# Performance work log

Measured on AMD Instinct MI355X. Metric: run time of the kernel, lower is better.

Reference implementation:

```python
import jax, jax.numpy as jnp
import numpy as np
from jax import lax

I, H, O, S = 1024, 1024, 32000, 2048


def setup_inputs() -> dict:
    key = jax.random.key(0)
    ks = jax.random.split(key, 7)
    s = 1.0 / np.sqrt(H)
    return {
        "x": jax.random.normal(ks[0], (1, S, I), jnp.float32),
        "W_ih": jax.random.uniform(ks[1], (H, I), jnp.float32, -s, s),
        "W_hh": jax.random.uniform(ks[2], (H, H), jnp.float32, -s, s),
        "b_ih": jax.random.uniform(ks[3], (H,), jnp.float32, -s, s),
        "b_hh": jax.random.uniform(ks[4], (H,), jnp.float32, -s, s),
        "W_fc": jax.random.uniform(ks[5], (O, H), jnp.float32, -s, s),
        "b_fc": jax.random.uniform(ks[6], (O,), jnp.float32, -s, s),
    }


def reference(x, W_ih, W_hh, b_ih, b_hh, W_fc, b_fc):
    # Precompute input projection for all timesteps in one GEMM: [s, H]
    xp = jnp.einsum('si,hi->sh', x[0], W_ih) + b_ih + b_hh
    h0 = jnp.zeros((W_hh.shape[0],), x.dtype)

    def step(h, xt):
        h_new = jnp.tanh(xt + h @ W_hh.T)
        return h_new, h_new

    _, hs = lax.scan(step, h0, xp)  # hs: [s, H]
    # Linear head over all timesteps: [s, O]
    return hs @ W_fc.T + b_fc
```

## Files before the change

### kernel.cpp

```cpp
#include <hip/hip_runtime.h>
#include <math.h>

typedef _Float16 f16;
typedef f16 f16x2 __attribute__((ext_vector_type(2)));
typedef f16 f16x4 __attribute__((ext_vector_type(4)));
typedef f16 f16x8 __attribute__((ext_vector_type(8)));
typedef float f32x4 __attribute__((ext_vector_type(4)));

#define HDIM 1024
#define SEQ  2048
#define NBLK 16
#define NGWK 240
#define RPB  64
#define NTIL 4000

__global__ void k_clear(unsigned long long* __restrict__ p, int n,
                        unsigned* __restrict__ sR, int nr,
                        unsigned* __restrict__ sG, int ng) {
  int stride = gridDim.x * blockDim.x;
  int id = blockIdx.x * blockDim.x + threadIdx.x;
  for (int i = id; i < n; i += stride) p[i] = 0ULL;
  for (int i = id; i < nr; i += stride) sR[i] = 0u;
  for (int i = id; i < ng; i += stride) sG[i] = 0u;
}

__global__ void k_cvt(const float* __restrict__ in, f16* __restrict__ out, int n4) {
  int stride = gridDim.x * blockDim.x;
  for (int i = blockIdx.x * blockDim.x + threadIdx.x; i < n4; i += stride) {
    float4 v = ((const float4*)in)[i];
    f16x4 o = { (f16)v.x, (f16)v.y, (f16)v.z, (f16)v.w };
    ((f16x4*)out)[i] = o;
  }
}

__global__ void k_bias(const float* __restrict__ a, const float* __restrict__ b,
                       float* __restrict__ o) {
  int i = blockIdx.x * blockDim.x + threadIdx.x;
  if (i < HDIM) o[i] = a[i] + b[i];
}

__global__ __launch_bounds__(256) void k_gemm(
    const f16* __restrict__ A, const f16* __restrict__ B,
    const float* __restrict__ bias, float* __restrict__ C, int N)
{
  const int K = 1024;
  __shared__ __align__(16) f16 lsA[128 * 32];
  __shared__ __align__(16) f16 lsB[128 * 32];
  const int tid = threadIdx.x;
  const int l   = tid & 63;
  const int wv  = tid >> 6;
  const int mb  = blockIdx.y * 128;
  const int nb  = blockIdx.x * 128;
  const int wm  = (wv >> 1) * 64;
  const int wn  = (wv & 1) * 64;

  f32x4 acc[4][4] = {};

  for (int kt = 0; kt < K; kt += 32) {
    uint4 ra[2], rb[2];
#pragma unroll
    for (int i = 0; i < 2; ++i) {
      int c = tid + i * 256;
      int row = c >> 2, off = (c & 3) * 8;
      ra[i] = *(const uint4*)(A + (size_t)(mb + row) * K + kt + off);
      rb[i] = *(const uint4*)(B + (size_t)(nb + row) * K + kt + off);
    }
    __syncthreads();
#pragma unroll
    for (int i = 0; i < 2; ++i) {
      int c = tid + i * 256;
      *(uint4*)(lsA + c * 8) = ra[i];
      *(uint4*)(lsB + c * 8) = rb[i];
    }
    __syncthreads();

    f16x8 af[4], bf[4];
#pragma unroll
    for (int m = 0; m < 4; ++m)
      af[m] = *(const f16x8*)(lsA + (wm + m * 16 + (l & 15)) * 32 + (l >> 4) * 8);
#pragma unroll
    for (int n = 0; n < 4; ++n)
      bf[n] = *(const f16x8*)(lsB + (wn + n * 16 + (l & 15)) * 32 + (l >> 4) * 8);
#pragma unroll
    for (int m = 0; m < 4; ++m)
#pragma unroll
      for (int n = 0; n < 4; ++n)
        acc[m][n] = __builtin_amdgcn_mfma_f32_16x16x32_f16(af[m], bf[n], acc[m][n], 0, 0, 0);
  }

#pragma unroll
  for (int n = 0; n < 4; ++n) {
    int col = nb + wn + n * 16 + (l & 15);
    float bv = bias[col];
#pragma unroll
    for (int m = 0; m < 4; ++m) {
#pragma unroll
      for (int j = 0; j < 4; ++j) {
        int row = mb + wm + m * 16 + (l >> 4) * 4 + j;
        C[(size_t)row * N + col] = acc[m][n][j] + bv;
      }
    }
  }
}

__device__ __forceinline__ void pub64(unsigned long long* p, unsigned long long v) {
  (void)__hip_atomic_exchange(p, v, __ATOMIC_RELAXED, __HIP_MEMORY_SCOPE_AGENT);
}
__device__ __forceinline__ void pub32(unsigned* p, unsigned v) {
  (void)__hip_atomic_exchange(p, v, __ATOMIC_RELAXED, __HIP_MEMORY_SCOPE_AGENT);
}
__device__ __forceinline__ unsigned long long rd64(const unsigned long long* p) {
  return __hip_atomic_fetch_add((unsigned long long*)p, 0ULL,
                                __ATOMIC_RELAXED, __HIP_MEMORY_SCOPE_AGENT);
}
__device__ __forceinline__ unsigned rd32(const unsigned* p) {
  return __hip_atomic_fetch_add((unsigned*)p, 0u,
                                __ATOMIC_RELAXED, __HIP_MEMORY_SCOPE_AGENT);
}

__global__ __launch_bounds__(1024, 4) void k_main(
    const float* __restrict__ W,
    const float* __restrict__ xp,
    unsigned long long* __restrict__ pairs,
    unsigned* __restrict__ sumR,
    unsigned* __restrict__ sumG,
    f16* __restrict__ hs,
    const f16* __restrict__ Wfc,
    const float* __restrict__ bfc,
    float* __restrict__ out)
{
  __shared__ unsigned hl[544];
  __shared__ int s_dead;
  __shared__ __align__(16) f16 lsA[128 * 32];
  __shared__ __align__(16) f16 lsB[128 * 32];

  const int tid = threadIdx.x;
  const int l   = tid & 63;
  const int wv  = tid >> 6;

  if (blockIdx.x < NBLK) {
    const int b   = blockIdx.x;
    const int w   = wv;
    const int hfl = l >> 5;
    const int ch  = l & 31;
    const int r0  = b * RPB + w * 4 + hfl * 2;
    const int c0  = ch * 32;

    if (tid == 0) s_dead = 0;

    f16x2 wv0[16], wv1[16];
    {
      const float* w0 = W + (size_t)r0 * HDIM + c0;
      const float* w1 = w0 + HDIM;
#pragma unroll
      for (int j = 0; j < 16; ++j) {
        wv0[j] = f16x2{ (f16)w0[2 * j], (f16)w0[2 * j + 1] };
        wv1[j] = f16x2{ (f16)w1[2 * j], (f16)w1[2 * j + 1] };
      }
    }

    for (unsigned t = 1; t <= SEQ; ++t) {
      float x0 = 0.f, x1 = 0.f;
      if (ch == 0) {
        const float* xr = xp + (size_t)(t - 1) * HDIM + r0;
        x0 = xr[0]; x1 = xr[1];
      }

      if (w == 0) {
        const unsigned need = t - 1;
        {
          int g = 0;
          for (;;) {
            unsigned sv = need;
            if (l < 16) sv = rd32(sumR + l * 32);
            if (__ballot(sv < need) == 0ULL) break;
            if (++g > (1 << 20)) { if (l == 0) s_dead = 1; break; }
          }
        }
        {
          const unsigned long long* row = pairs + ((t - 1) & 1) * 512 + l * 8;
          unsigned long long u[8];
          int g = 0;
          for (;;) {
            bool ok = true;
#pragma unroll
            for (int j = 0; j < 8; ++j) u[j] = rd64(row + j);
#pragma unroll
            for (int j = 0; j < 8; ++j)
              ok &= ((unsigned)(u[j] >> 32) == (t - 1));
            if (__ballot(!ok) == 0ULL) break;
            if (++g > (1 << 20)) { if (l == 0) s_dead = 1; break; }
          }
          const int base = (l >> 1) * 17 + (l & 1) * 8;
#pragma unroll
          for (int j = 0; j < 8; ++j) hl[base + j] = (unsigned)u[j];
        }
      }
      __syncthreads();
      if (s_dead) return;

      float s0 = 0.f, s1 = 0.f;
#pragma unroll
      for (int j = 0; j < 16; ++j) {
        f16x2 hv = __builtin_bit_cast(f16x2, hl[ch * 17 + j]);
        s0 = __builtin_amdgcn_fdot2(wv0[j], hv, s0, false);
        s1 = __builtin_amdgcn_fdot2(wv1[j], hv, s1, false);
      }
#pragma unroll
      for (int m = 16; m >= 1; m >>= 1) {
        s0 += __shfl_xor(s0, m, 64);
        s1 += __shfl_xor(s1, m, 64);
      }

      if (ch == 0) {
        float a0 = x0 + s0, a1 = x1 + s1;
        float e0 = __expf(2.f * a0), e1 = __expf(2.f * a1);
        float h0 = 1.f - 2.f * __builtin_amdgcn_rcpf(e0 + 1.f);
        float h1 = 1.f - 2.f * __builtin_amdgcn_rcpf(e1 + 1.f);
        f16x2 hh = { (f16)h0, (f16)h1 };
        unsigned pay = __builtin_bit_cast(unsigned, hh);
        unsigned long long val = ((unsigned long long)t << 32) | (unsigned long long)pay;
        pub64(pairs + (t & 1) * 512 + (r0 >> 1), val);
        pub32((unsigned*)hs + (((size_t)t * HDIM + r0) >> 1), pay);
      }

      __syncthreads();
      if (tid == 0) {
        pub32(sumR + b * 32, t);
        pub32(sumG + (size_t)t * 16 + b, t);
      }
    }
    return;
  }

  const int g  = blockIdx.x - NBLK;
  const int wm = (wv >> 2) * 32;
  const int wn = (wv & 3) * 32;
  const int half = tid >> 9;
  const int i    = tid & 511;
  const int srow = i >> 2;
  const int soff = (i & 3) * 8;

  for (int ti = g; ti < NTIL; ti += NGWK) {
    const int mt = ti / 250, nt = ti % 250;
    const unsigned S = (unsigned)(mt * 128 + 128);

    if (wv == 0) {
      const unsigned* sp = sumG + (size_t)S * 16 + l;
      int gu = 0;
      for (;;) {
        unsigned sv = S;
        if (l < 16) sv = rd32(sp);
        if (__ballot(sv < S) == 0ULL) break;
        __builtin_amdgcn_s_sleep(32);
        if (++gu > (1 << 21)) break;
      }
    }
    __syncthreads();

    const f16* A = hs + (size_t)(mt * 128 + 1) * HDIM;
    const f16* B = Wfc + (size_t)nt * 128 * HDIM;
    const f16* sbase = (half ? B : A) + (size_t)srow * HDIM + soff;

    f32x4 acc[2][2] = {};

    for (int kt = 0; kt < HDIM; kt += 32) {
      uint4 r = *(const uint4*)(sbase + kt);
      __syncthreads();
      *(uint4*)((half ? lsB : lsA) + i * 8) = r;
      __syncthreads();

      f16x8 af[2], bf[2];
#pragma unroll
      for (int m = 0; m < 2; ++m)
        af[m] = *(const f16x8*)(lsA + (wm + m * 16 + (l & 15)) * 32 + (l >> 4) * 8);
#pragma unroll
      for (int n = 0; n < 2; ++n)
        bf[n] = *(const f16x8*)(lsB + (wn + n * 16 + (l & 15)) * 32 + (l >> 4) * 8);
#pragma unroll
      for (int m = 0; m < 2; ++m)
#pragma unroll
        for (int n = 0; n < 2; ++n)
          acc[m][n] = __builtin_amdgcn_mfma_f32_16x16x32_f16(af[m], bf[n], acc[m][n], 0, 0, 0);
    }

#pragma unroll
    for (int n = 0; n < 2; ++n) {
      int col = nt * 128 + wn + n * 16 + (l & 15);
      float bv = bfc[col];
#pragma unroll
      for (int m = 0; m < 2; ++m) {
#pragma unroll
        for (int j = 0; j < 4; ++j) {
          int row = mt * 128 + wm + m * 16 + (l >> 4) * 4 + j;
          out[(size_t)row * 32000 + col] = acc[m][n][j] + bv;
        }
      }
    }
    __syncthreads();
  }
}

extern "C" void kernel_launch(void* const* d_in, const int* in_sizes, int n_in,
                              void* d_out, int out_size, void* d_ws, size_t ws_size,
                              hipStream_t stream) {
  const float* x    = (const float*)d_in[0];
  const float* W_ih = (const float*)d_in[1];
  const float* W_hh = (const float*)d_in[2];
  const float* b_ih = (const float*)d_in[3];
  const float* b_hh = (const float*)d_in[4];
  const float* W_fc = (const float*)d_in[5];
  const float* b_fc = (const float*)d_in[6];
  float* out = (float*)d_out;

  char* ws = (char*)d_ws;
  unsigned long long* pairs = (unsigned long long*)ws;
  unsigned* sumR  = (unsigned*)(ws + 8192);
  unsigned* sumG  = (unsigned*)(ws + 10240);
  f16*   hs16  = (f16*)(ws + 141376);
  float* xp    = (float*)(ws + 4337728);
  f16*   x16   = (f16*)(ws + 12726336);
  f16*   wih16 = (f16*)(ws + 16920640);
  f16*   wfc16 = (f16*)(ws + 19017792);
  float* bsum  = (float*)(ws + 84553792);

  k_clear<<<256, 256, 0, stream>>>(pairs, 2 * 512, sumR, 16 * 32,
                                   sumG, (SEQ + 1) * 16);
  k_cvt<<<1024, 256, 0, stream>>>(x, x16, 2048 * 1024 / 4);
  k_cvt<<<1024, 256, 0, stream>>>(W_ih, wih16, 1024 * 1024 / 4);
  k_cvt<<<2048, 256, 0, stream>>>(W_fc, wfc16, 32000 * 1024 / 4);
  k_bias<<<4, 256, 0, stream>>>(b_ih, b_hh, bsum);

  k_gemm<<<dim3(8, 16), 256, 0, stream>>>(x16, wih16, bsum, xp, 1024);

  k_main<<<NBLK + NGWK, 1024, 0, stream>>>(W_hh, xp, pairs, sumR, sumG, hs16,
                                           wfc16, b_fc, out);
}
```

Baseline: 4.643 ms.

## Drop per-step round barrier, double-buffer LDS state, coarsen head-GEMM signaling

```diff
diff --git a/kernel.cpp b/kernel.cpp
--- a/kernel.cpp
+++ b/kernel.cpp
@@ -15,12 +15,10 @@
 #define NTIL 4000
 
 __global__ void k_clear(unsigned long long* __restrict__ p, int n,
-                        unsigned* __restrict__ sR, int nr,
                         unsigned* __restrict__ sG, int ng) {
   int stride = gridDim.x * blockDim.x;
   int id = blockIdx.x * blockDim.x + threadIdx.x;
   for (int i = id; i < n; i += stride) p[i] = 0ULL;
-  for (int i = id; i < nr; i += stride) sR[i] = 0u;
   for (int i = id; i < ng; i += stride) sG[i] = 0u;
 }
 
@@ -122,14 +120,13 @@
     const float* __restrict__ W,
     const float* __restrict__ xp,
     unsigned long long* __restrict__ pairs,
-    unsigned* __restrict__ sumR,
     unsigned* __restrict__ sumG,
     f16* __restrict__ hs,
     const f16* __restrict__ Wfc,
     const float* __restrict__ bfc,
     float* __restrict__ out)
 {
-  __shared__ unsigned hl[544];
+  __shared__ unsigned hl[2 * 544];
   __shared__ int s_dead;
   __shared__ __align__(16) f16 lsA[128 * 32];
   __shared__ __align__(16) f16 lsB[128 * 32];
@@ -160,6 +157,7 @@
     }
 
     for (unsigned t = 1; t <= SEQ; ++t) {
+      const int hb = (int)(t & 1) * 544;
       float x0 = 0.f, x1 = 0.f;
       if (ch == 0) {
         const float* xr = xp + (size_t)(t - 1) * HDIM + r0;
@@ -167,34 +165,23 @@
       }
 
       if (w == 0) {
+        const unsigned long long* row = pairs + ((t - 1) & 1) * 512 + l * 8;
         const unsigned need = t - 1;
-        {
-          int g = 0;
-          for (;;) {
-            unsigned sv = need;
-            if (l < 16) sv = rd32(sumR + l * 32);
-            if (__ballot(sv < need) == 0ULL) break;
-            if (++g > (1 << 20)) { if (l == 0) s_dead = 1; break; }
-          }
+        unsigned long long u[8];
+        int g = 0;
+        for (;;) {
+          bool ok = true;
+#pragma unroll
+          for (int j = 0; j < 8; ++j) u[j] = rd64(row + j);
+#pragma unroll
+          for (int j = 0; j < 8; ++j)
+            ok &= ((unsigned)(u[j] >> 32) == need);
+          if (__ballot(!ok) == 0ULL) break;
+          if (++g > (1 << 20)) { if (l == 0) s_dead = 1; break; }
         }
-        {
-          const unsigned long long* row = pairs + ((t - 1) & 1) * 512 + l * 8;
-          unsigned long long u[8];
-          int g = 0;
-          for (;;) {
-            bool ok = true;
-#pragma unroll
-            for (int j = 0; j < 8; ++j) u[j] = rd64(row + j);
-#pragma unroll
-            for (int j = 0; j < 8; ++j)
-              ok &= ((unsigned)(u[j] >> 32) == (t - 1));
-            if (__ballot(!ok) == 0ULL) break;
-            if (++g > (1 << 20)) { if (l == 0) s_dead = 1; break; }
-          }
-          const int base = (l >> 1) * 17 + (l & 1) * 8;
-#pragma unroll
-          for (int j = 0; j < 8; ++j) hl[base + j] = (unsigned)u[j];
-        }
+        const int base = (l >> 1) * 17 + (l & 1) * 8;
+#pragma unroll
+        for (int j = 0; j < 8; ++j) hl[hb + base + j] = (unsigned)u[j];
       }
       __syncthreads();
       if (s_dead) return;
@@ -202,7 +189,7 @@
       float s0 = 0.f, s1 = 0.f;
 #pragma unroll
       for (int j = 0; j < 16; ++j) {
-        f16x2 hv = __builtin_bit_cast(f16x2, hl[ch * 17 + j]);
+        f16x2 hv = __builtin_bit_cast(f16x2, hl[hb + ch * 17 + j]);
         s0 = __builtin_amdgcn_fdot2(wv0[j], hv, s0, false);
         s1 = __builtin_amdgcn_fdot2(wv1[j], hv, s1, false);
       }
@@ -224,10 +211,10 @@
         pub32((unsigned*)hs + (((size_t)t * HDIM + r0) >> 1), pay);
       }
 
-      __syncthreads();
-      if (tid == 0) {
-        pub32(sumR + b * 32, t);
-        pub32(sumG + (size_t)t * 16 + b, t);
+      if ((t & 127u) == 0u) {
+        __syncthreads();
+        if (tid == 0)
+          pub32(sumG + (int)((t >> 7) - 1) * 16 + b, t);
       }
     }
     return;
@@ -246,7 +233,7 @@
     const unsigned S = (unsigned)(mt * 128 + 128);
 
     if (wv == 0) {
-      const unsigned* sp = sumG + (size_t)S * 16 + l;
+      const unsigned* sp = sumG + mt * 16 + l;
       int gu = 0;
       for (;;) {
         unsigned sv = S;
@@ -315,17 +302,15 @@
 
   char* ws = (char*)d_ws;
   unsigned long long* pairs = (unsigned long long*)ws;
-  unsigned* sumR  = (unsigned*)(ws + 8192);
-  unsigned* sumG  = (unsigned*)(ws + 10240);
-  f16*   hs16  = (f16*)(ws + 141376);
-  float* xp    = (float*)(ws + 4337728);
-  f16*   x16   = (f16*)(ws + 12726336);
-  f16*   wih16 = (f16*)(ws + 16920640);
-  f16*   wfc16 = (f16*)(ws + 19017792);
-  float* bsum  = (float*)(ws + 84553792);
-
-  k_clear<<<256, 256, 0, stream>>>(pairs, 2 * 512, sumR, 16 * 32,
-                                   sumG, (SEQ + 1) * 16);
+  unsigned* sumG  = (unsigned*)(ws + 8192);
+  f16*   hs16  = (f16*)(ws + 16384);
+  float* xp    = (float*)(ws + 4212736);
+  f16*   x16   = (f16*)(ws + 12601344);
+  f16*   wih16 = (f16*)(ws + 16795648);
+  f16*   wfc16 = (f16*)(ws + 18892800);
+  float* bsum  = (float*)(ws + 84428800);
+
+  k_clear<<<4, 256, 0, stream>>>(pairs, 2 * 512, sumG, 16 * 16);
   k_cvt<<<1024, 256, 0, stream>>>(x, x16, 2048 * 1024 / 4);
   k_cvt<<<1024, 256, 0, stream>>>(W_ih, wih16, 1024 * 1024 / 4);
   k_cvt<<<2048, 256, 0, stream>>>(W_fc, wfc16, 32000 * 1024 / 4);
@@ -333,6 +318,6 @@
 
   k_gemm<<<dim3(8, 16), 256, 0, stream>>>(x16, wih16, bsum, xp, 1024);
 
-  k_main<<<NBLK + NGWK, 1024, 0, stream>>>(W_hh, xp, pairs, sumR, sumG, hs16,
+  k_main<<<NBLK + NGWK, 1024, 0, stream>>>(W_hh, xp, pairs, sumG, hs16,
                                            wfc16, b_fc, out);
 }
```

New measurement: 4.793 ms. 1.03x slower.

## Halve recurrent blocks, assigning four hidden rows per half-wave

Applied to the files above, without the earlier changes.

```diff
diff --git a/kernel.cpp b/kernel.cpp
--- a/kernel.cpp
+++ b/kernel.cpp
@@ -9,9 +9,9 @@
 
 #define HDIM 1024
 #define SEQ  2048
-#define NBLK 16
-#define NGWK 240
-#define RPB  64
+#define NBLK 8
+#define NGWK 248
+#define RPB  128
 #define NTIL 4000
 
 __global__ void k_clear(unsigned long long* __restrict__ p, int n,
@@ -143,27 +143,31 @@
     const int w   = wv;
     const int hfl = l >> 5;
     const int ch  = l & 31;
-    const int r0  = b * RPB + w * 4 + hfl * 2;
+    const int r0  = b * RPB + w * 8 + hfl * 4;
     const int c0  = ch * 32;
 
     if (tid == 0) s_dead = 0;
 
-    f16x2 wv0[16], wv1[16];
+    f16x2 wv0[16], wv1[16], wv2[16], wv3[16];
     {
       const float* w0 = W + (size_t)r0 * HDIM + c0;
       const float* w1 = w0 + HDIM;
+      const float* w2 = w0 + 2 * HDIM;
+      const float* w3 = w0 + 3 * HDIM;
 #pragma unroll
       for (int j = 0; j < 16; ++j) {
         wv0[j] = f16x2{ (f16)w0[2 * j], (f16)w0[2 * j + 1] };
         wv1[j] = f16x2{ (f16)w1[2 * j], (f16)w1[2 * j + 1] };
+        wv2[j] = f16x2{ (f16)w2[2 * j], (f16)w2[2 * j + 1] };
+        wv3[j] = f16x2{ (f16)w3[2 * j], (f16)w3[2 * j + 1] };
       }
     }
 
     for (unsigned t = 1; t <= SEQ; ++t) {
-      float x0 = 0.f, x1 = 0.f;
+      float x0 = 0.f, x1 = 0.f, x2 = 0.f, x3 = 0.f;
       if (ch == 0) {
         const float* xr = xp + (size_t)(t - 1) * HDIM + r0;
-        x0 = xr[0]; x1 = xr[1];
+        x0 = xr[0]; x1 = xr[1]; x2 = xr[2]; x3 = xr[3];
       }
 
       if (w == 0) {
@@ -172,7 +176,7 @@
           int g = 0;
           for (;;) {
             unsigned sv = need;
-            if (l < 16) sv = rd32(sumR + l * 32);
+            if (l < NBLK) sv = rd32(sumR + l * 32);
             if (__ballot(sv < need) == 0ULL) break;
             if (++g > (1 << 20)) { if (l == 0) s_dead = 1; break; }
           }
@@ -199,29 +203,42 @@
       __syncthreads();
       if (s_dead) return;
 
-      float s0 = 0.f, s1 = 0.f;
+      float s0 = 0.f, s1 = 0.f, s2 = 0.f, s3 = 0.f;
 #pragma unroll
       for (int j = 0; j < 16; ++j) {
         f16x2 hv = __builtin_bit_cast(f16x2, hl[ch * 17 + j]);
         s0 = __builtin_amdgcn_fdot2(wv0[j], hv, s0, false);
         s1 = __builtin_amdgcn_fdot2(wv1[j], hv, s1, false);
+        s2 = __builtin_amdgcn_fdot2(wv2[j], hv, s2, false);
+        s3 = __builtin_amdgcn_fdot2(wv3[j], hv, s3, false);
       }
 #pragma unroll
       for (int m = 16; m >= 1; m >>= 1) {
         s0 += __shfl_xor(s0, m, 64);
         s1 += __shfl_xor(s1, m, 64);
+        s2 += __shfl_xor(s2, m, 64);
+        s3 += __shfl_xor(s3, m, 64);
       }
 
       if (ch == 0) {
-        float a0 = x0 + s0, a1 = x1 + s1;
+        float a0 = x0 + s0, a1 = x1 + s1, a2 = x2 + s2, a3 = x3 + s3;
         float e0 = __expf(2.f * a0), e1 = __expf(2.f * a1);
+        float e2 = __expf(2.f * a2), e3 = __expf(2.f * a3);
         float h0 = 1.f - 2.f * __builtin_amdgcn_rcpf(e0 + 1.f);
         float h1 = 1.f - 2.f * __builtin_amdgcn_rcpf(e1 + 1.f);
-        f16x2 hh = { (f16)h0, (f16)h1 };
-        unsigned pay = __builtin_bit_cast(unsigned, hh);
-        unsigned long long val = ((unsigned long long)t << 32) | (unsigned long long)pay;
-        pub64(pairs + (t & 1) * 512 + (r0 >> 1), val);
-        pub32((unsigned*)hs + (((size_t)t * HDIM + r0) >> 1), pay);
+        float h2 = 1.f - 2.f * __builtin_amdgcn_rcpf(e2 + 1.f);
+        float h3 = 1.f - 2.f * __builtin_amdgcn_rcpf(e3 + 1.f);
+        f16x2 hh01 = { (f16)h0, (f16)h1 };
+        f16x2 hh23 = { (f16)h2, (f16)h3 };
+        unsigned p01 = __builtin_bit_cast(unsigned, hh01);
+        unsigned p23 = __builtin_bit_cast(unsigned, hh23);
+        unsigned long long tg = (unsigned long long)t << 32;
+        unsigned long long* slot = pairs + (t & 1) * 512 + (r0 >> 1);
+        pub64(slot,     tg | (unsigned long long)p01);
+        pub64(slot + 1, tg | (unsigned long long)p23);
+        unsigned* hp = (unsigned*)hs + (((size_t)t * HDIM + r0) >> 1);
+        pub32(hp,     p01);
+        pub32(hp + 1, p23);
       }
 
       __syncthreads();
@@ -250,7 +267,7 @@
       int gu = 0;
       for (;;) {
         unsigned sv = S;
-        if (l < 16) sv = rd32(sp);
+        if (l < NBLK) sv = rd32(sp);
         if (__ballot(sv < S) == 0ULL) break;
         __builtin_amdgcn_s_sleep(32);
         if (++gu > (1 << 21)) break;
@@ -324,7 +341,7 @@
   f16*   wfc16 = (f16*)(ws + 19017792);
   float* bsum  = (float*)(ws + 84553792);
 
-  k_clear<<<256, 256, 0, stream>>>(pairs, 2 * 512, sumR, 16 * 32,
+  k_clear<<<256, 256, 0, stream>>>(pairs, 2 * 512, sumR, 8 * 32,
                                    sumG, (SEQ + 1) * 16);
   k_cvt<<<1024, 256, 0, stream>>>(x, x16, 2048 * 1024 / 4);
   k_cvt<<<1024, 256, 0, stream>>>(W_ih, wih16, 1024 * 1024 / 4);
```

After: 5.810 ms. 25.1% more time.
